# Optimization experiments

Hardware: AMD Instinct MI355X
Metric: run time of the kernel (lower is better)

Reference implementation:

```python
import jax, jax.numpy as jnp
import numpy as np

NUM_HEADS = 16

def _rope_tables(T, head_dim):
    # angular_freq: (1/1024)**linspace(0,1,head_dim//4), padded with head_dim//4 zeros
    af = (1.0 / 1024.0) ** jnp.linspace(0.0, 1.0, head_dim // 4, dtype=jnp.float32)
    af = jnp.concatenate([af, jnp.zeros(head_dim // 4, dtype=jnp.float32)])  # [head_dim//2]
    t = jnp.arange(T, dtype=jnp.float32)
    theta = t[:, None] * af[None, :]  # [T, head_dim//2]
    return jnp.cos(theta), jnp.sin(theta)

def _apply_rope(x_bthd, cos, sin):
    # x_bthd: [B,T,H,D]; cos/sin: [T,D//2]
    x1, x2 = jnp.split(x_bthd.astype(jnp.float32), 2, axis=-1)
    c = cos[None, :, None, :]
    s = sin[None, :, None, :]
    y1 = x1 * c + x2 * s
    y2 = -x1 * s + x2 * c
    return jnp.concatenate([y1, y2], axis=-1).astype(x_bthd.dtype)

def setup_inputs() -> dict:
    key = jax.random.key(0)
    k1, k2, k3 = jax.random.split(key, 3)
    B, T, C = 4, 2048, 1024
    std = 0.5 * C ** (-0.5)
    bound = (3.0 ** 0.5) * std
    x = jax.random.normal(k1, (B, T, C), dtype=jnp.float32)
    qkv_w = jax.random.uniform(k2, (3, C, C), dtype=jnp.float32, minval=-bound, maxval=bound)
    c_proj_w = 0.02 * jax.random.normal(k3, (C, C), dtype=jnp.float32)
    c_proj_b = jnp.zeros((C,), dtype=jnp.float32)
    return {"x": x, "qkv_w": qkv_w, "c_proj_w": c_proj_w, "c_proj_b": c_proj_b}

def reference(x, qkv_w, c_proj_w, c_proj_b):
    B, T, C = x.shape
    H = NUM_HEADS
    D = C // H
    # QKV projection: F.linear(x, qkv_w.flatten(end_dim=1)) -> x @ W.T
    qkv = jnp.einsum('btc,nc->btn', x, qkv_w.reshape(3 * C, C))  # [B,T,3C]
    qkv = qkv.reshape(B, T, 3 * H, D)
    q, k, v = jnp.split(qkv, 3, axis=-2)  # each [B,T,H,D]
    cos, sin = _rope_tables(T, D)
    q = _apply_rope(q, cos, sin)
    k = _apply_rope(k, cos, sin)
    # causal SDPA, scale 1/sqrt(D)
    scale = 1.0 / jnp.sqrt(jnp.float32(D))
    scores = jnp.einsum('bqhd,bkhd->bhqk', q, k) * scale  # [B,H,T,T]
    mask = jnp.tril(jnp.ones((T, T), dtype=bool))
    scores = jnp.where(mask[None, None], scores, jnp.finfo(scores.dtype).min)
    attn = jax.nn.softmax(scores, axis=-1)
    y = jnp.einsum('bhqk,bkhd->bqhd', attn, v).reshape(B, T, C)
    return y @ c_proj_w.T + c_proj_b
```

## Files before the change

kernel.cpp:

```cpp
#include <hip/hip_runtime.h>

typedef unsigned short ushort_t;
typedef __bf16 bf16x8 __attribute__((ext_vector_type(8)));
typedef unsigned short ushort8_t __attribute__((ext_vector_type(8)));
typedef unsigned short ushort4_t __attribute__((ext_vector_type(4)));
typedef float floatx4 __attribute__((ext_vector_type(4)));
typedef unsigned int uint4_t __attribute__((ext_vector_type(4)));
typedef unsigned int uint2_t __attribute__((ext_vector_type(2)));

__device__ __forceinline__ ushort_t f2bf(float f) {
    unsigned int u = __float_as_uint(f);
    u += 0x7FFFu + ((u >> 16) & 1u);
    return (ushort_t)(u >> 16);
}
__device__ __forceinline__ float bf2f(ushort_t b) {
    return __uint_as_float(((unsigned int)b) << 16);
}
__device__ __forceinline__ bf16x8 ld_frag(const ushort_t* p) {
    ushort8_t u = *(const ushort8_t*)p;
    return __builtin_bit_cast(bf16x8, u);
}
__device__ __forceinline__ unsigned pack_trunc(float lo, float hi) {
    return __builtin_amdgcn_perm(__float_as_uint(hi), __float_as_uint(lo), 0x07060302u);
}
__device__ __forceinline__ floatx4 mfma16(bf16x8 a, bf16x8 b, floatx4 c) {
    return __builtin_amdgcn_mfma_f32_16x16x32_bf16(a, b, c, 0, 0, 0);
}
__device__ __forceinline__ void async16(const ushort_t* g, ushort_t* l) {
    __builtin_amdgcn_global_load_lds((const __attribute__((address_space(1))) void*)g,
                                     (__attribute__((address_space(3))) void*)l, 16, 0, 0);
}

__global__ __launch_bounds__(256) void cvt_dual(const float* __restrict__ s1,
                                                ushort_t* __restrict__ d1, int n1,
                                                const float* __restrict__ s2,
                                                ushort_t* __restrict__ d2, int n2) {
    int idx = blockIdx.x * 256 + threadIdx.x;
    const float* src;
    ushort_t* dst;
    if (idx < n1) {
        src = s1; dst = d1;
    } else {
        idx -= n1;
        if (idx >= n2) return;
        src = s2; dst = d2;
    }
    const float4* s = (const float4*)src + (size_t)idx * 2;
    float4 a = s[0], b = s[1];
    ushort8_t v;
    v[0] = f2bf(a.x); v[1] = f2bf(a.y); v[2] = f2bf(a.z); v[3] = f2bf(a.w);
    v[4] = f2bf(b.x); v[5] = f2bf(b.y); v[6] = f2bf(b.z); v[7] = f2bf(b.w);
    *(ushort8_t*)(dst + (size_t)idx * 8) = v;
}

template <int MODE>
__global__ __launch_bounds__(256) void gemm_a(const ushort_t* __restrict__ A,
                                              const ushort_t* __restrict__ B,
                                              const float* __restrict__ bias,
                                              void* __restrict__ Cout,
                                              ushort_t* __restrict__ vt,
                                              int M, int N) {
    constexpr int K = 1024;
    __shared__ __attribute__((aligned(16))) ushort_t As[128 * 32];
    __shared__ __attribute__((aligned(16))) ushort_t Bs[128 * 32];
    const int tid = threadIdx.x;
    const int lane = tid & 63, wave = tid >> 6;
    const int quad = lane >> 4, l16 = lane & 15;
    const int wm = wave & 1, wn = wave >> 1;
    const int m0 = blockIdx.y * 128, n0 = blockIdx.x * 128;

    const ushort_t* ga = A + (size_t)(m0 + wave * 32 + (lane >> 2)) * K + (lane & 3) * 8;
    const ushort_t* gb = B + (size_t)(n0 + wave * 32 + (lane >> 2)) * K + (lane & 3) * 8;
    const ushort_t* ga2 = ga + 16 * K;
    const ushort_t* gb2 = gb + 16 * K;
    ushort_t* la = As + wave * 1024;
    ushort_t* lb = Bs + wave * 1024;

    floatx4 acc[4][4] = {};

#pragma unroll
    for (int k0 = 0; k0 < K; k0 += 32) {
        __syncthreads();
        async16(ga + k0, la);
        async16(ga2 + k0, la + 512);
        async16(gb + k0, lb);
        async16(gb2 + k0, lb + 512);
        __syncthreads();

        bf16x8 af[4], bfr[4];
#pragma unroll
        for (int mt = 0; mt < 4; ++mt)
            af[mt] = ld_frag(&As[(wm * 64 + mt * 16 + l16) * 32 + quad * 8]);
#pragma unroll
        for (int nt = 0; nt < 4; ++nt)
            bfr[nt] = ld_frag(&Bs[(wn * 64 + nt * 16 + l16) * 32 + quad * 8]);
#pragma unroll
        for (int mt = 0; mt < 4; ++mt)
#pragma unroll
            for (int nt = 0; nt < 4; ++nt)
                acc[mt][nt] = mfma16(af[mt], bfr[nt], acc[mt][nt]);
    }

    if constexpr (MODE == 2) {
        if (n0 + wn * 64 < 2048) {
            float afreq = exp2f((float)l16 * (-10.0f / 15.0f));
#pragma unroll
            for (int mt = 0; mt < 4; ++mt) {
                int rowb = m0 + wm * 64 + mt * 16 + quad * 4;
#pragma unroll
                for (int r = 0; r < 4; ++r) {
                    int t = (rowb + r) & 2047;
                    float th = (float)t * afreq;
                    float sn, cs;
                    __sincosf(th, &sn, &cs);
                    float q1 = acc[mt][0][r], q2 = acc[mt][2][r];
                    acc[mt][0][r] = q1 * cs + q2 * sn;
                    acc[mt][2][r] = -q1 * sn + q2 * cs;
                }
            }
        }
    }

#pragma unroll
    for (int mt = 0; mt < 4; ++mt) {
        int row = m0 + wm * 64 + mt * 16 + quad * 4;
#pragma unroll
        for (int nt = 0; nt < 4; ++nt) {
            int nglob = n0 + wn * 64 + nt * 16 + l16;
            if constexpr (MODE == 0) {
                float bv = bias ? bias[nglob] : 0.0f;
#pragma unroll
                for (int r = 0; r < 4; ++r)
                    ((float*)Cout)[(size_t)(row + r) * N + nglob] = acc[mt][nt][r] + bv;
            } else {
                if (nglob < 2048) {
#pragma unroll
                    for (int r = 0; r < 4; ++r)
                        ((ushort_t*)Cout)[(size_t)(row + r) * 2048 + nglob] =
                            f2bf(acc[mt][nt][r]);
                } else {
                    int d = nglob & 63, hh = (nglob >> 6) & 15;
                    int bb = row >> 11, t = row & 2047;
                    ushort4_t pk;
                    pk.x = f2bf(acc[mt][nt][0]);
                    pk.y = f2bf(acc[mt][nt][1]);
                    pk.z = f2bf(acc[mt][nt][2]);
                    pk.w = f2bf(acc[mt][nt][3]);
                    *(ushort4_t*)&vt[(((size_t)bb * 16 + hh) * 64 + d) * 2048 + t] = pk;
                }
            }
        }
    }
}

#define ATT_SCALE 0.18033688011112042f

template <bool DIAG>
__device__ __forceinline__ void attn_step(
    const ushort_t* __restrict__ Ks, const ushort_t* __restrict__ Vt,
    ushort_t* __restrict__ Pw, const bf16x8 (&qf)[2][2],
    floatx4 (&o)[2][4], floatx4 (&lac)[2], float (&m_)[2],
    int quad, int l16, int sw8, int mhi, int qrel) {
    ushort8_t ou;
#pragma unroll
    for (int j = 0; j < 8; ++j) ou[j] = 0x3F80;
    const bf16x8 vONE = __builtin_bit_cast(bf16x8, ou);

    floatx4 s[8][2];
#pragma unroll
    for (int mt = 0; mt < 8; ++mt) {
        if (DIAG && mt > mhi) continue;
        const ushort_t* kr = &Ks[(mt * 16 + l16) * 64];
        bf16x8 k0 = ld_frag(kr + ((quad * 8) ^ sw8));
        bf16x8 k1 = ld_frag(kr + ((32 + quad * 8) ^ sw8));
#pragma unroll
        for (int nt = 0; nt < 2; ++nt) {
            floatx4 z = {};
            z = mfma16(k0, qf[nt][0], z);
            s[mt][nt] = mfma16(k1, qf[nt][1], z);
        }
    }
    if (DIAG) {
#pragma unroll
        for (int mt = 0; mt < 8; ++mt) {
            if (mt > mhi) continue;
#pragma unroll
            for (int nt = 0; nt < 2; ++nt)
#pragma unroll
                for (int r = 0; r < 4; ++r)
                    if (mt * 16 + quad * 4 + r > qrel + nt * 16 + l16)
                        s[mt][nt][r] = -3e38f;
        }
    }
    float alpha_l[2];
#pragma unroll
    for (int nt = 0; nt < 2; ++nt) {
        float mx = -3e38f;
#pragma unroll
        for (int mt = 0; mt < 8; ++mt) {
            if (DIAG && mt > mhi) continue;
            mx = fmaxf(mx, fmaxf(fmaxf(s[mt][nt][0], s[mt][nt][1]),
                                 fmaxf(s[mt][nt][2], s[mt][nt][3])));
        }
        mx = fmaxf(mx, __shfl_xor(mx, 16));
        mx = fmaxf(mx, __shfl_xor(mx, 32));
        float mnew = fmaxf(m_[nt], mx);
        alpha_l[nt] = __builtin_amdgcn_exp2f(m_[nt] - mnew);
        m_[nt] = mnew;
#pragma unroll
        for (int mt = 0; mt < 8; ++mt) {
            if (DIAG && mt > mhi) continue;
#pragma unroll
            for (int r = 0; r < 4; ++r)
                s[mt][nt][r] = __builtin_amdgcn_exp2f(s[mt][nt][r] - mnew);
        }
    }
#pragma unroll
    for (int mtq = 0; mtq < 2; ++mtq)
#pragma unroll
        for (int r = 0; r < 4; ++r) {
            float ao = __shfl(alpha_l[mtq], quad * 4 + r);
            lac[mtq][r] *= ao;
#pragma unroll
            for (int ntd = 0; ntd < 4; ++ntd) o[mtq][ntd][r] *= ao;
        }
#pragma unroll
    for (int mt = 0; mt < 8; ++mt) {
        if (DIAG && mt > mhi) continue;
#pragma unroll
        for (int nt = 0; nt < 2; ++nt) {
            uint2_t pk;
            pk.x = pack_trunc(s[mt][nt][0], s[mt][nt][1]);
            pk.y = pack_trunc(s[mt][nt][2], s[mt][nt][3]);
            *(uint2_t*)&Pw[(nt * 16 + l16) * 136 + mt * 16 + quad * 4] = pk;
        }
    }
#pragma unroll
    for (int kc = 0; kc < 4; ++kc) {
        if (DIAG && kc > (mhi >> 1)) continue;
        bf16x8 ap0 = ld_frag(&Pw[l16 * 136 + kc * 32 + quad * 8]);
        bf16x8 ap1 = ld_frag(&Pw[(16 + l16) * 136 + kc * 32 + quad * 8]);
        lac[0] = mfma16(ap0, vONE, lac[0]);
        lac[1] = mfma16(ap1, vONE, lac[1]);
#pragma unroll
        for (int ntd = 0; ntd < 4; ++ntd) {
            bf16x8 bv = ld_frag(&Vt[(ntd * 16 + l16) * 136 + kc * 32 + quad * 8]);
            o[0][ntd] = mfma16(ap0, bv, o[0][ntd]);
            o[1][ntd] = mfma16(ap1, bv, o[1][ntd]);
        }
    }
}

__global__ __launch_bounds__(256, 2) void attn_kernel(const ushort_t* __restrict__ qk,
                                                      const ushort_t* __restrict__ vt,
                                                      ushort_t* __restrict__ y) {
    __shared__ __attribute__((aligned(16))) ushort_t lds[34304];
    ushort_t* Ks = lds;
    ushort_t* Vt = lds + 8192;
    ushort_t* Pw0 = lds + 16896;

    const int tid = threadIdx.x, lane = tid & 63, w = tid >> 6;
    const int quad = lane >> 4, l16 = lane & 15;
    const int lrow = lane >> 3, lchunk = lane & 7;
    const int sw8 = 8 * (l16 >> 1);
    const int bh = (int)blockIdx.x >> 3, j = (int)blockIdx.x & 7;
    const int b = bh >> 4, h = bh & 15;
    ushort_t* Pw = Pw0 + w * 4352;

    const ushort_t* base_k = qk + (size_t)(b * 2048) * 2048 + 1024 + h * 64;
    const ushort_t* base_v = vt + (size_t)bh * 64 * 2048;
    const int vd = w * 4 + (lane >> 4);
    const int vc8 = lane & 15;

    ushort8_t kreg[4], vreg[4];
    auto load_kv = [&](int kt) {
        const ushort_t* gk = base_k + (size_t)(kt * 128) * 2048 + lchunk * 8;
#pragma unroll
        for (int i = 0; i < 4; ++i)
            kreg[i] = *(const ushort8_t*)(gk + (size_t)(w * 32 + i * 8 + lrow) * 2048);
        const ushort_t* gv = base_v + kt * 128;
#pragma unroll
        for (int i = 0; i < 4; ++i)
            vreg[i] = *(const ushort8_t*)(gv + (size_t)(i * 16 + vd) * 2048 + vc8 * 8);
    };
    auto store_kv = [&]() {
#pragma unroll
        for (int i = 0; i < 4; ++i) {
            int row = w * 32 + i * 8 + lrow;
            *(ushort8_t*)&Ks[row * 64 + 8 * (lchunk ^ ((row >> 1) & 7))] = kreg[i];
        }
#pragma unroll
        for (int i = 0; i < 4; ++i)
            *(ushort8_t*)&Vt[(i * 16 + vd) * 136 + vc8 * 8] = vreg[i];
    };

#pragma unroll 1
    for (int ph = 0; ph < 2; ++ph) {
        const int jj = ph ? (15 - j) : j;
        const int q0 = jj * 128 + w * 32;

        bf16x8 qf[2][2];
        {
            const ushort_t* qb = qk + (size_t)(b * 2048 + q0) * 2048 + h * 64 + quad * 8;
#pragma unroll
            for (int nt = 0; nt < 2; ++nt)
#pragma unroll
                for (int kd = 0; kd < 2; ++kd) {
                    ushort8_t raw =
                        *(const ushort8_t*)(qb + (size_t)(nt * 16 + l16) * 2048 + kd * 32);
                    uint4_t dw;
#pragma unroll
                    for (int jx = 0; jx < 4; ++jx) {
                        float f0 = bf2f(raw[2 * jx]) * ATT_SCALE;
                        float f1 = bf2f(raw[2 * jx + 1]) * ATT_SCALE;
                        dw[jx] = pack_trunc(f0, f1);
                    }
                    qf[nt][kd] = __builtin_bit_cast(bf16x8, dw);
                }
        }

        floatx4 o[2][4] = {};
        floatx4 lac[2] = {};
        float m_[2] = {-3e38f, -3e38f};

        load_kv(0);
#pragma unroll 1
        for (int kt = 0; kt <= jj; ++kt) {
            __syncthreads();
            store_kv();
            __syncthreads();
            if (kt < jj) load_kv(kt + 1);

            if (kt < jj)
                attn_step<false>(Ks, Vt, Pw, qf, o, lac, m_, quad, l16, sw8, 7, 0);
            else
                attn_step<true>(Ks, Vt, Pw, qf, o, lac, m_, quad, l16, sw8,
                                2 * w + 1, w * 32);
        }

        ushort_t* yb = y + (size_t)(b * 2048 + q0) * 1024 + h * 64;
#pragma unroll
        for (int mtq = 0; mtq < 2; ++mtq)
#pragma unroll
            for (int r = 0; r < 4; ++r) {
                float inv = 1.0f / lac[mtq][r];
                int row = mtq * 16 + quad * 4 + r;
#pragma unroll
                for (int ntd = 0; ntd < 4; ++ntd)
                    yb[(size_t)row * 1024 + ntd * 16 + l16] = f2bf(o[mtq][ntd][r] * inv);
            }
    }
}

extern "C" void kernel_launch(void* const* d_in, const int* in_sizes, int n_in,
                              void* d_out, int out_size, void* d_ws, size_t ws_size,
                              hipStream_t stream) {
    const float* x = (const float*)d_in[0];
    const float* qkv_w = (const float*)d_in[1];
    const float* c_proj_w = (const float*)d_in[2];
    const float* c_proj_b = (const float*)d_in[3];
    float* out = (float*)d_out;

    const int M = 8192;

    ushort_t* qk = (ushort_t*)d_ws;
    ushort_t* vt = (ushort_t*)((char*)d_ws + (size_t)33554432);
    ushort_t* wpb = vt;
    ushort_t* wb = (ushort_t*)((char*)d_ws + (size_t)50331648);
    ushort_t* y = wb;
    ushort_t* xb = (ushort_t*)d_out;

    cvt_dual<<<dim3(5632), 256, 0, stream>>>(x, xb, M * 1024 / 8,
                                             qkv_w, wb, 3072 * 1024 / 8);

    gemm_a<2><<<dim3(3072 / 128, M / 128), 256, 0, stream>>>(
        xb, wb, nullptr, qk, vt, M, 3072);

    attn_kernel<<<dim3(512), 256, 0, stream>>>(qk, vt, y);

    cvt_dual<<<dim3(512), 256, 0, stream>>>(c_proj_w, wpb, 1024 * 1024 / 8,
                                            nullptr, nullptr, 0);

    gemm_a<0><<<dim3(1024 / 128, M / 128), 256, 0, stream>>>(
        y, wpb, c_proj_b, out, nullptr, M, 1024);
}
```

Measured before the change: 257.2 us.

## Load K/V fragments directly from global memory, drop LDS staging and barriers

The attention kernel no longer stages K and V tiles through shared memory with block-wide barriers. Each wave now loads its MFMA fragments straight from global memory (relying on L1/L2 for reuse across the four waves). The change also skips the online-softmax rescale of O and l unless the running max grows by more than a threshold, and raises wave priority around the MFMA blocks. The cost is redundant global/L2 traffic per wave, more registers for the prefetched fragments, and strided uncoalesced loads.

```diff
diff --git a/kernel.cpp b/kernel.cpp
--- a/kernel.cpp
+++ b/kernel.cpp
@@ -157,29 +157,49 @@
 
 template <bool DIAG>
 __device__ __forceinline__ void attn_step(
-    const ushort_t* __restrict__ Ks, const ushort_t* __restrict__ Vt,
+    const ushort_t* __restrict__ kg,
+    const ushort_t* __restrict__ vg,
     ushort_t* __restrict__ Pw, const bf16x8 (&qf)[2][2],
     floatx4 (&o)[2][4], floatx4 (&lac)[2], float (&m_)[2],
-    int quad, int l16, int sw8, int mhi, int qrel) {
+    int quad, int l16, int mhi, int qrel) {
     ushort8_t ou;
 #pragma unroll
     for (int j = 0; j < 8; ++j) ou[j] = 0x3F80;
     const bf16x8 vONE = __builtin_bit_cast(bf16x8, ou);
 
-    floatx4 s[8][2];
+    bf16x8 kf0[8], kf1[8];
 #pragma unroll
     for (int mt = 0; mt < 8; ++mt) {
         if (DIAG && mt > mhi) continue;
-        const ushort_t* kr = &Ks[(mt * 16 + l16) * 64];
-        bf16x8 k0 = ld_frag(kr + ((quad * 8) ^ sw8));
-        bf16x8 k1 = ld_frag(kr + ((32 + quad * 8) ^ sw8));
+        const ushort_t* kr = kg + (size_t)(mt * 16 + l16) * 2048 + quad * 8;
+        kf0[mt] = ld_frag(kr);
+        kf1[mt] = ld_frag(kr + 32);
+    }
+
+    floatx4 s[8][2];
+    __builtin_amdgcn_s_setprio(1);
+#pragma unroll
+    for (int mt = 0; mt < 8; ++mt) {
+        if (DIAG && mt > mhi) continue;
 #pragma unroll
         for (int nt = 0; nt < 2; ++nt) {
             floatx4 z = {};
-            z = mfma16(k0, qf[nt][0], z);
-            s[mt][nt] = mfma16(k1, qf[nt][1], z);
-        }
-    }
+            z = mfma16(kf0[mt], qf[nt][0], z);
+            s[mt][nt] = mfma16(kf1[mt], qf[nt][1], z);
+        }
+    }
+    __builtin_amdgcn_s_setprio(0);
+
+    bf16x8 vf[4][4];
+#pragma unroll
+    for (int kc = 0; kc < 4; ++kc) {
+        if (DIAG && kc > (mhi >> 1)) continue;
+#pragma unroll
+        for (int ntd = 0; ntd < 4; ++ntd)
+            vf[kc][ntd] =
+                ld_frag(vg + (size_t)(ntd * 16 + l16) * 2048 + kc * 32 + quad * 8);
+    }
+
     if (DIAG) {
 #pragma unroll
         for (int mt = 0; mt < 8; ++mt) {
@@ -192,38 +212,51 @@
                         s[mt][nt][r] = -3e38f;
         }
     }
-    float alpha_l[2];
+
+    float mx[2];
 #pragma unroll
     for (int nt = 0; nt < 2; ++nt) {
-        float mx = -3e38f;
+        float m0 = -3e38f;
 #pragma unroll
         for (int mt = 0; mt < 8; ++mt) {
             if (DIAG && mt > mhi) continue;
-            mx = fmaxf(mx, fmaxf(fmaxf(s[mt][nt][0], s[mt][nt][1]),
+            m0 = fmaxf(m0, fmaxf(fmaxf(s[mt][nt][0], s[mt][nt][1]),
                                  fmaxf(s[mt][nt][2], s[mt][nt][3])));
         }
-        mx = fmaxf(mx, __shfl_xor(mx, 16));
-        mx = fmaxf(mx, __shfl_xor(mx, 32));
-        float mnew = fmaxf(m_[nt], mx);
-        alpha_l[nt] = __builtin_amdgcn_exp2f(m_[nt] - mnew);
-        m_[nt] = mnew;
+        m0 = fmaxf(m0, __shfl_xor(m0, 16));
+        m0 = fmaxf(m0, __shfl_xor(m0, 32));
+        mx[nt] = m0;
+    }
+    bool resc =
+        !__all((mx[0] - m_[0] <= 8.0f) && (mx[1] - m_[1] <= 8.0f));
+    if (resc) {
+        float alpha_l[2];
+#pragma unroll
+        for (int nt = 0; nt < 2; ++nt) {
+            float mnew = fmaxf(m_[nt], mx[nt]);
+            alpha_l[nt] = __builtin_amdgcn_exp2f(m_[nt] - mnew);
+            m_[nt] = mnew;
+        }
+#pragma unroll
+        for (int mtq = 0; mtq < 2; ++mtq)
+#pragma unroll
+            for (int r = 0; r < 4; ++r) {
+                float ao = __shfl(alpha_l[mtq], quad * 4 + r);
+                lac[mtq][r] *= ao;
+#pragma unroll
+                for (int ntd = 0; ntd < 4; ++ntd) o[mtq][ntd][r] *= ao;
+            }
+    }
+#pragma unroll
+    for (int nt = 0; nt < 2; ++nt)
 #pragma unroll
         for (int mt = 0; mt < 8; ++mt) {
             if (DIAG && mt > mhi) continue;
 #pragma unroll
             for (int r = 0; r < 4; ++r)
-                s[mt][nt][r] = __builtin_amdgcn_exp2f(s[mt][nt][r] - mnew);
-        }
-    }
-#pragma unroll
-    for (int mtq = 0; mtq < 2; ++mtq)
-#pragma unroll
-        for (int r = 0; r < 4; ++r) {
-            float ao = __shfl(alpha_l[mtq], quad * 4 + r);
-            lac[mtq][r] *= ao;
-#pragma unroll
-            for (int ntd = 0; ntd < 4; ++ntd) o[mtq][ntd][r] *= ao;
-        }
+                s[mt][nt][r] = __builtin_amdgcn_exp2f(s[mt][nt][r] - m_[nt]);
+        }
+
 #pragma unroll
     for (int mt = 0; mt < 8; ++mt) {
         if (DIAG && mt > mhi) continue;
@@ -235,6 +268,8 @@
             *(uint2_t*)&Pw[(nt * 16 + l16) * 136 + mt * 16 + quad * 4] = pk;
         }
     }
+
+    __builtin_amdgcn_s_setprio(1);
 #pragma unroll
     for (int kc = 0; kc < 4; ++kc) {
         if (DIAG && kc > (mhi >> 1)) continue;
@@ -244,55 +279,26 @@
         lac[1] = mfma16(ap1, vONE, lac[1]);
 #pragma unroll
         for (int ntd = 0; ntd < 4; ++ntd) {
-            bf16x8 bv = ld_frag(&Vt[(ntd * 16 + l16) * 136 + kc * 32 + quad * 8]);
-            o[0][ntd] = mfma16(ap0, bv, o[0][ntd]);
-            o[1][ntd] = mfma16(ap1, bv, o[1][ntd]);
-        }
-    }
+            o[0][ntd] = mfma16(ap0, vf[kc][ntd], o[0][ntd]);
+            o[1][ntd] = mfma16(ap1, vf[kc][ntd], o[1][ntd]);
+        }
+    }
+    __builtin_amdgcn_s_setprio(0);
 }
 
 __global__ __launch_bounds__(256, 2) void attn_kernel(const ushort_t* __restrict__ qk,
                                                       const ushort_t* __restrict__ vt,
                                                       ushort_t* __restrict__ y) {
-    __shared__ __attribute__((aligned(16))) ushort_t lds[34304];
-    ushort_t* Ks = lds;
-    ushort_t* Vt = lds + 8192;
-    ushort_t* Pw0 = lds + 16896;
+    __shared__ __attribute__((aligned(16))) ushort_t Pw_all[4 * 4352];
 
     const int tid = threadIdx.x, lane = tid & 63, w = tid >> 6;
     const int quad = lane >> 4, l16 = lane & 15;
-    const int lrow = lane >> 3, lchunk = lane & 7;
-    const int sw8 = 8 * (l16 >> 1);
     const int bh = (int)blockIdx.x >> 3, j = (int)blockIdx.x & 7;
     const int b = bh >> 4, h = bh & 15;
-    ushort_t* Pw = Pw0 + w * 4352;
+    ushort_t* Pw = Pw_all + w * 4352;
 
     const ushort_t* base_k = qk + (size_t)(b * 2048) * 2048 + 1024 + h * 64;
     const ushort_t* base_v = vt + (size_t)bh * 64 * 2048;
-    const int vd = w * 4 + (lane >> 4);
-    const int vc8 = lane & 15;
-
-    ushort8_t kreg[4], vreg[4];
-    auto load_kv = [&](int kt) {
-        const ushort_t* gk = base_k + (size_t)(kt * 128) * 2048 + lchunk * 8;
-#pragma unroll
-        for (int i = 0; i < 4; ++i)
-            kreg[i] = *(const ushort8_t*)(gk + (size_t)(w * 32 + i * 8 + lrow) * 2048);
-        const ushort_t* gv = base_v + kt * 128;
-#pragma unroll
-        for (int i = 0; i < 4; ++i)
-            vreg[i] = *(const ushort8_t*)(gv + (size_t)(i * 16 + vd) * 2048 + vc8 * 8);
-    };
-    auto store_kv = [&]() {
-#pragma unroll
-        for (int i = 0; i < 4; ++i) {
-            int row = w * 32 + i * 8 + lrow;
-            *(ushort8_t*)&Ks[row * 64 + 8 * (lchunk ^ ((row >> 1) & 7))] = kreg[i];
-        }
-#pragma unroll
-        for (int i = 0; i < 4; ++i)
-            *(ushort8_t*)&Vt[(i * 16 + vd) * 136 + vc8 * 8] = vreg[i];
-    };
 
 #pragma unroll 1
     for (int ph = 0; ph < 2; ++ph) {
@@ -323,19 +329,15 @@
         floatx4 lac[2] = {};
         float m_[2] = {-3e38f, -3e38f};
 
-        load_kv(0);
 #pragma unroll 1
         for (int kt = 0; kt <= jj; ++kt) {
-            __syncthreads();
-            store_kv();
-            __syncthreads();
-            if (kt < jj) load_kv(kt + 1);
-
+            const ushort_t* kg = base_k + (size_t)(kt * 128) * 2048;
+            const ushort_t* vg = base_v + kt * 128;
             if (kt < jj)
-                attn_step<false>(Ks, Vt, Pw, qf, o, lac, m_, quad, l16, sw8, 7, 0);
+                attn_step<false>(kg, vg, Pw, qf, o, lac, m_, quad, l16, 7, 0);
             else
-                attn_step<true>(Ks, Vt, Pw, qf, o, lac, m_, quad, l16, sw8,
-                                2 * w + 1, w * 32);
+                attn_step<true>(kg, vg, Pw, qf, o, lac, m_, quad, l16, 2 * w + 1,
+                                w * 32);
         }
 
         ushort_t* yb = y + (size_t)(b * 2048 + q0) * 1024 + h * 64;
```

New measurement: 312.4 us. 1.21x slower.

## Keep P in registers via permlane swaps, add lazy rescale and restructure attention grid

Applied to the files above, without the earlier changes.

The attention kernel stops staging the softmax probabilities through LDS. It repacks them in registers with permlane32/permlane16 swaps into the MFMA A-operand layout, which frees LDS so launch bounds can rise to 4 blocks per CU. The online-softmax rescale of o and lac is skipped unless some row max grows by more than 8 (log2 units). The grid now uses one block per (query tile, head) instead of two paired phases, ordered heavy-first by a lookup table, and MFMA sections are wrapped in s_setprio. Risks include register pressure at the higher occupancy target and a changed load balance across the grid.

```diff
diff --git a/kernel.cpp b/kernel.cpp
--- a/kernel.cpp
+++ b/kernel.cpp
@@ -29,6 +29,12 @@
 __device__ __forceinline__ void async16(const ushort_t* g, ushort_t* l) {
     __builtin_amdgcn_global_load_lds((const __attribute__((address_space(1))) void*)g,
                                      (__attribute__((address_space(3))) void*)l, 16, 0, 0);
+}
+__device__ __forceinline__ void pl32swap(unsigned& a, unsigned& b) {
+    asm volatile("v_permlane32_swap_b32 %0, %1" : "+v"(a), "+v"(b));
+}
+__device__ __forceinline__ void pl16swap(unsigned& a, unsigned& b) {
+    asm volatile("v_permlane16_swap_b32 %0, %1" : "+v"(a), "+v"(b));
 }
 
 __global__ __launch_bounds__(256) void cvt_dual(const float* __restrict__ s1,
@@ -158,8 +164,7 @@
 template <bool DIAG>
 __device__ __forceinline__ void attn_step(
     const ushort_t* __restrict__ Ks, const ushort_t* __restrict__ Vt,
-    ushort_t* __restrict__ Pw, const bf16x8 (&qf)[2][2],
-    floatx4 (&o)[2][4], floatx4 (&lac)[2], float (&m_)[2],
+    const bf16x8 (&qf)[2][2], floatx4 (&o)[2][4], floatx4 (&lac)[2], float (&m_)[2],
     int quad, int l16, int sw8, int mhi, int qrel) {
     ushort8_t ou;
 #pragma unroll
@@ -167,6 +172,7 @@
     const bf16x8 vONE = __builtin_bit_cast(bf16x8, ou);
 
     floatx4 s[8][2];
+    __builtin_amdgcn_s_setprio(1);
 #pragma unroll
     for (int mt = 0; mt < 8; ++mt) {
         if (DIAG && mt > mhi) continue;
@@ -180,6 +186,8 @@
             s[mt][nt] = mfma16(k1, qf[nt][1], z);
         }
     }
+    __builtin_amdgcn_s_setprio(0);
+
     if (DIAG) {
 #pragma unroll
         for (int mt = 0; mt < 8; ++mt) {
@@ -192,80 +200,105 @@
                         s[mt][nt][r] = -3e38f;
         }
     }
-    float alpha_l[2];
+
+    float mx[2];
 #pragma unroll
     for (int nt = 0; nt < 2; ++nt) {
-        float mx = -3e38f;
+        float m0 = -3e38f;
 #pragma unroll
         for (int mt = 0; mt < 8; ++mt) {
             if (DIAG && mt > mhi) continue;
-            mx = fmaxf(mx, fmaxf(fmaxf(s[mt][nt][0], s[mt][nt][1]),
+            m0 = fmaxf(m0, fmaxf(fmaxf(s[mt][nt][0], s[mt][nt][1]),
                                  fmaxf(s[mt][nt][2], s[mt][nt][3])));
         }
-        mx = fmaxf(mx, __shfl_xor(mx, 16));
-        mx = fmaxf(mx, __shfl_xor(mx, 32));
-        float mnew = fmaxf(m_[nt], mx);
-        alpha_l[nt] = __builtin_amdgcn_exp2f(m_[nt] - mnew);
-        m_[nt] = mnew;
+        m0 = fmaxf(m0, __shfl_xor(m0, 16));
+        m0 = fmaxf(m0, __shfl_xor(m0, 32));
+        mx[nt] = m0;
+    }
+    bool resc = !__all((mx[0] - m_[0] <= 8.0f) && (mx[1] - m_[1] <= 8.0f));
+    if (resc) {
+        float alpha_l[2];
+#pragma unroll
+        for (int nt = 0; nt < 2; ++nt) {
+            float mnew = fmaxf(m_[nt], mx[nt]);
+            alpha_l[nt] = __builtin_amdgcn_exp2f(m_[nt] - mnew);
+            m_[nt] = mnew;
+        }
+#pragma unroll
+        for (int mtq = 0; mtq < 2; ++mtq)
+#pragma unroll
+            for (int r = 0; r < 4; ++r) {
+                float ao = __shfl(alpha_l[mtq], quad * 4 + r);
+                lac[mtq][r] *= ao;
+#pragma unroll
+                for (int ntd = 0; ntd < 4; ++ntd) o[mtq][ntd][r] *= ao;
+            }
+    }
+#pragma unroll
+    for (int nt = 0; nt < 2; ++nt)
 #pragma unroll
         for (int mt = 0; mt < 8; ++mt) {
             if (DIAG && mt > mhi) continue;
 #pragma unroll
             for (int r = 0; r < 4; ++r)
-                s[mt][nt][r] = __builtin_amdgcn_exp2f(s[mt][nt][r] - mnew);
-        }
-    }
-#pragma unroll
-    for (int mtq = 0; mtq < 2; ++mtq)
-#pragma unroll
-        for (int r = 0; r < 4; ++r) {
-            float ao = __shfl(alpha_l[mtq], quad * 4 + r);
-            lac[mtq][r] *= ao;
-#pragma unroll
-            for (int ntd = 0; ntd < 4; ++ntd) o[mtq][ntd][r] *= ao;
-        }
-#pragma unroll
-    for (int mt = 0; mt < 8; ++mt) {
-        if (DIAG && mt > mhi) continue;
-#pragma unroll
-        for (int nt = 0; nt < 2; ++nt) {
-            uint2_t pk;
-            pk.x = pack_trunc(s[mt][nt][0], s[mt][nt][1]);
-            pk.y = pack_trunc(s[mt][nt][2], s[mt][nt][3]);
-            *(uint2_t*)&Pw[(nt * 16 + l16) * 136 + mt * 16 + quad * 4] = pk;
-        }
-    }
+                s[mt][nt][r] = __builtin_amdgcn_exp2f(s[mt][nt][r] - m_[nt]);
+        }
+
+    uint2_t pk[2][8];
+#pragma unroll
+    for (int nt = 0; nt < 2; ++nt)
+#pragma unroll
+        for (int mt = 0; mt < 8; ++mt) {
+            if (DIAG && mt > mhi) continue;
+            pk[nt][mt].x = pack_trunc(s[mt][nt][0], s[mt][nt][1]);
+            pk[nt][mt].y = pack_trunc(s[mt][nt][2], s[mt][nt][3]);
+        }
+
+    __builtin_amdgcn_s_setprio(1);
 #pragma unroll
     for (int kc = 0; kc < 4; ++kc) {
         if (DIAG && kc > (mhi >> 1)) continue;
-        bf16x8 ap0 = ld_frag(&Pw[l16 * 136 + kc * 32 + quad * 8]);
-        bf16x8 ap1 = ld_frag(&Pw[(16 + l16) * 136 + kc * 32 + quad * 8]);
-        lac[0] = mfma16(ap0, vONE, lac[0]);
-        lac[1] = mfma16(ap1, vONE, lac[1]);
+        bf16x8 ap[2];
+#pragma unroll
+        for (int nt = 0; nt < 2; ++nt) {
+            unsigned a0 = pk[nt][2 * kc].x, a1 = pk[nt][2 * kc].y;
+            unsigned b0 = pk[nt][2 * kc + 1].x, b1 = pk[nt][2 * kc + 1].y;
+            pl32swap(a0, b0);
+            pl16swap(a0, b0);
+            pl32swap(a1, b1);
+            pl16swap(a1, b1);
+            uint4_t ud;
+            ud[0] = a0; ud[1] = a1; ud[2] = b0; ud[3] = b1;
+            ap[nt] = __builtin_bit_cast(bf16x8, ud);
+        }
+        lac[0] = mfma16(ap[0], vONE, lac[0]);
+        lac[1] = mfma16(ap[1], vONE, lac[1]);
 #pragma unroll
         for (int ntd = 0; ntd < 4; ++ntd) {
             bf16x8 bv = ld_frag(&Vt[(ntd * 16 + l16) * 136 + kc * 32 + quad * 8]);
-            o[0][ntd] = mfma16(ap0, bv, o[0][ntd]);
-            o[1][ntd] = mfma16(ap1, bv, o[1][ntd]);
-        }
-    }
-}
-
-__global__ __launch_bounds__(256, 2) void attn_kernel(const ushort_t* __restrict__ qk,
+            o[0][ntd] = mfma16(ap[0], bv, o[0][ntd]);
+            o[1][ntd] = mfma16(ap[1], bv, o[1][ntd]);
+        }
+    }
+    __builtin_amdgcn_s_setprio(0);
+}
+
+__global__ __launch_bounds__(256, 4) void attn_kernel(const ushort_t* __restrict__ qk,
                                                       const ushort_t* __restrict__ vt,
                                                       ushort_t* __restrict__ y) {
-    __shared__ __attribute__((aligned(16))) ushort_t lds[34304];
-    ushort_t* Ks = lds;
-    ushort_t* Vt = lds + 8192;
-    ushort_t* Pw0 = lds + 16896;
+    __shared__ __attribute__((aligned(16))) ushort_t Ks[128 * 64];
+    __shared__ __attribute__((aligned(16))) ushort_t Vt[64 * 136];
 
     const int tid = threadIdx.x, lane = tid & 63, w = tid >> 6;
     const int quad = lane >> 4, l16 = lane & 15;
     const int lrow = lane >> 3, lchunk = lane & 7;
     const int sw8 = 8 * (l16 >> 1);
-    const int bh = (int)blockIdx.x >> 3, j = (int)blockIdx.x & 7;
+
+    const int idx = (int)blockIdx.x;
+    const int rank = idx >> 6, bh = idx & 63;
+    constexpr int jj_tab[16] = {15, 13, 11, 9, 0, 2, 4, 6, 14, 12, 10, 8, 1, 3, 5, 7};
+    const int jj = jj_tab[rank];
     const int b = bh >> 4, h = bh & 15;
-    ushort_t* Pw = Pw0 + w * 4352;
 
     const ushort_t* base_k = qk + (size_t)(b * 2048) * 2048 + 1024 + h * 64;
     const ushort_t* base_v = vt + (size_t)bh * 64 * 2048;
@@ -294,62 +327,57 @@
             *(ushort8_t*)&Vt[(i * 16 + vd) * 136 + vc8 * 8] = vreg[i];
     };
 
+    const int q0 = jj * 128 + w * 32;
+
+    bf16x8 qf[2][2];
+    {
+        const ushort_t* qb = qk + (size_t)(b * 2048 + q0) * 2048 + h * 64 + quad * 8;
+#pragma unroll
+        for (int nt = 0; nt < 2; ++nt)
+#pragma unroll
+            for (int kd = 0; kd < 2; ++kd) {
+                ushort8_t raw =
+                    *(const ushort8_t*)(qb + (size_t)(nt * 16 + l16) * 2048 + kd * 32);
+                uint4_t dw;
+#pragma unroll
+                for (int jx = 0; jx < 4; ++jx) {
+                    float f0 = bf2f(raw[2 * jx]) * ATT_SCALE;
+                    float f1 = bf2f(raw[2 * jx + 1]) * ATT_SCALE;
+                    dw[jx] = pack_trunc(f0, f1);
+                }
+                qf[nt][kd] = __builtin_bit_cast(bf16x8, dw);
+            }
+    }
+
+    floatx4 o[2][4] = {};
+    floatx4 lac[2] = {};
+    float m_[2] = {-3e38f, -3e38f};
+
+    load_kv(0);
 #pragma unroll 1
-    for (int ph = 0; ph < 2; ++ph) {
-        const int jj = ph ? (15 - j) : j;
-        const int q0 = jj * 128 + w * 32;
-
-        bf16x8 qf[2][2];
-        {
-            const ushort_t* qb = qk + (size_t)(b * 2048 + q0) * 2048 + h * 64 + quad * 8;
-#pragma unroll
-            for (int nt = 0; nt < 2; ++nt)
-#pragma unroll
-                for (int kd = 0; kd < 2; ++kd) {
-                    ushort8_t raw =
-                        *(const ushort8_t*)(qb + (size_t)(nt * 16 + l16) * 2048 + kd * 32);
-                    uint4_t dw;
-#pragma unroll
-                    for (int jx = 0; jx < 4; ++jx) {
-                        float f0 = bf2f(raw[2 * jx]) * ATT_SCALE;
-                        float f1 = bf2f(raw[2 * jx + 1]) * ATT_SCALE;
-                        dw[jx] = pack_trunc(f0, f1);
-                    }
-                    qf[nt][kd] = __builtin_bit_cast(bf16x8, dw);
-                }
-        }
-
-        floatx4 o[2][4] = {};
-        floatx4 lac[2] = {};
-        float m_[2] = {-3e38f, -3e38f};
-
-        load_kv(0);
-#pragma unroll 1
-        for (int kt = 0; kt <= jj; ++kt) {
-            __syncthreads();
-            store_kv();
-            __syncthreads();
-            if (kt < jj) load_kv(kt + 1);
-
-            if (kt < jj)
-                attn_step<false>(Ks, Vt, Pw, qf, o, lac, m_, quad, l16, sw8, 7, 0);
-            else
-                attn_step<true>(Ks, Vt, Pw, qf, o, lac, m_, quad, l16, sw8,
-                                2 * w + 1, w * 32);
-        }
-
-        ushort_t* yb = y + (size_t)(b * 2048 + q0) * 1024 + h * 64;
-#pragma unroll
-        for (int mtq = 0; mtq < 2; ++mtq)
-#pragma unroll
-            for (int r = 0; r < 4; ++r) {
-                float inv = 1.0f / lac[mtq][r];
-                int row = mtq * 16 + quad * 4 + r;
-#pragma unroll
-                for (int ntd = 0; ntd < 4; ++ntd)
-                    yb[(size_t)row * 1024 + ntd * 16 + l16] = f2bf(o[mtq][ntd][r] * inv);
-            }
-    }
+    for (int kt = 0; kt <= jj; ++kt) {
+        __syncthreads();
+        store_kv();
+        __syncthreads();
+        if (kt < jj) load_kv(kt + 1);
+
+        if (kt < jj)
+            attn_step<false>(Ks, Vt, qf, o, lac, m_, quad, l16, sw8, 7, 0);
+        else
+            attn_step<true>(Ks, Vt, qf, o, lac, m_, quad, l16, sw8, 2 * w + 1, w * 32);
+    }
+
+    ushort_t* yb = y + (size_t)(b * 2048 + q0) * 1024 + h * 64;
+#pragma unroll
+    for (int mtq = 0; mtq < 2; ++mtq)
+#pragma unroll
+        for (int r = 0; r < 4; ++r) {
+            float inv = 1.0f / lac[mtq][r];
+            int row = mtq * 16 + quad * 4 + r;
+#pragma unroll
+            for (int ntd = 0; ntd < 4; ++ntd)
+                yb[(size_t)row * 1024 + ntd * 16 + l16] = f2bf(o[mtq][ntd][r] * inv);
+        }
 }
 
 extern "C" void kernel_launch(void* const* d_in, const int* in_sizes, int n_in,
@@ -376,7 +404,7 @@
     gemm_a<2><<<dim3(3072 / 128, M / 128), 256, 0, stream>>>(
         xb, wb, nullptr, qk, vt, M, 3072);
 
-    attn_kernel<<<dim3(512), 256, 0, stream>>>(qk, vt, y);
+    attn_kernel<<<dim3(1024), 256, 0, stream>>>(qk, vt, y);
 
     cvt_dual<<<dim3(512), 256, 0, stream>>>(c_proj_w, wpb, 1024 * 1024 / 8,
                                             nullptr, nullptr, 0);
```

New measurement: 461.1 us. 79.3% more time.
